# Kernel optimization log

Measured on AMD Instinct MI355X. Metric: run time of the kernel, lower is better.

The kernel has to match this reference:

```python
import jax, jax.numpy as jnp
import numpy as np
from jax import lax

VOCAB = 5000
BLANK = 0          # vocab.unk_id
SMOOTHING = 0.1    # config.model.label_smoothing
ALPHA = 0.2        # config.model.alpha
NEG = -1e30        # finite stand-in for -inf (stable under logaddexp)


def setup_inputs() -> dict:
    key = jax.random.key(0)
    k1, k2, k3 = jax.random.split(key, 3)
    att_logits = jax.random.normal(k1, (16, 128, VOCAB), dtype=jnp.float32)
    ctc_logits = jax.random.normal(k2, (16, 512, VOCAB), dtype=jnp.float32)
    targets = jax.random.randint(k3, (16, 128), 0, VOCAB)
    return {"att_logits": att_logits, "ctc_logits": ctc_logits, "targets": targets}


def _label_smoothing_loss(logit_bsv, targets_bs):
    # torch: label_smoothed filled with smoothing/(V-1), confidence at target;
    # loss = mean over rows of sum(-label_smoothed * logit).
    B, S, V = logit_bsv.shape
    logit = logit_bsv.reshape(-1, V)                       # (B*S, V)
    tgt = targets_bs.reshape(-1)                           # (B*S,)
    confidence = 1.0 - SMOOTHING
    off = SMOOTHING / (V - 1)
    tgt_logit = jnp.take_along_axis(logit, tgt[:, None], axis=1)[:, 0]
    row_sum = jnp.sum(logit, axis=-1)
    # sum(-ls*logit) = -(confidence*logit[t] + off*(row_sum - logit[t]))
    per_row = -(confidence * tgt_logit + off * (row_sum - tgt_logit))
    return jnp.mean(per_row)


def _ctc_loss(log_probs_btv, targets_bs):
    # torch nn.CTCLoss(blank=BLANK, reduction='mean', zero_infinity=True)
    # input is time-major log-probs (T, B, V); full lengths on both sides.
    lp = jnp.transpose(log_probs_btv, (1, 0, 2))           # (T, B, V)
    T, B, V = lp.shape
    S = targets_bs.shape[1]
    L = 2 * S + 1
    # extended target: blank interleaved
    ext = jnp.full((B, L), BLANK, dtype=targets_bs.dtype).at[:, 1::2].set(targets_bs)
    # emission log-probs per extended symbol: (T, B, L)
    emit = jnp.take_along_axis(lp, jnp.broadcast_to(ext[None], (T, B, L)), axis=2)
    # skip (s-2) transition allowed when ext[s] != blank and ext[s] != ext[s-2]
    ext_m2 = jnp.roll(ext, 2, axis=1)
    allow2 = (ext != BLANK) & (ext != ext_m2)
    allow2 = allow2.at[:, :2].set(False)
    alpha0 = jnp.full((B, L), NEG, dtype=lp.dtype)
    alpha0 = alpha0.at[:, 0].set(emit[0, :, 0]).at[:, 1].set(emit[0, :, 1])

    negpad1 = jnp.full((B, 1), NEG, dtype=lp.dtype)
    negpad2 = jnp.full((B, 2), NEG, dtype=lp.dtype)

    def step(alpha, e_t):
        a1 = jnp.concatenate([negpad1, alpha[:, :-1]], axis=1)
        a2 = jnp.concatenate([negpad2, alpha[:, :-2]], axis=1)
        a2 = jnp.where(allow2, a2, NEG)
        new = jnp.logaddexp(jnp.logaddexp(alpha, a1), a2) + e_t
        return new, None

    alphaT, _ = lax.scan(step, alpha0, emit[1:])
    ll = jnp.logaddexp(alphaT[:, L - 1], alphaT[:, L - 2])
    loss_b = -ll                                           # (B,)
    # zero_infinity: invalid paths (loss ~ 1e30) -> 0
    loss_b = jnp.where(loss_b > 1e20, 0.0, loss_b)
    # reduction='mean': divide by target length, then mean over batch
    return jnp.mean(loss_b / S)


def reference(att_logits, ctc_logits, targets):
    att_loss = _label_smoothing_loss(att_logits, targets)
    ctc_loss = _ctc_loss(ctc_logits, targets)
    return ALPHA * att_loss + (1.0 - ALPHA) * ctc_loss
```

## Files before the change

### kernel.cpp

```cpp
#include <hip/hip_runtime.h>
#include <math.h>

#define VOCAB   5000
#define T_CTC   512
#define S_TGT   128
#define BATCH   16
#define ALPHA_W 0.2f
#define CONF    0.9f
#define OFFV    (0.1f / 4999.0f)
#define CSTR    132
#define ATT_N   (BATCH * S_TGT)
#define WS_OFF  4096
#define TCH     16
#define GATHER_BLKS (BATCH * (T_CTC / TCH))

__device__ __forceinline__ double dpp_shr1(double x)
{
    const int lo  = __double2loint(x);
    const int hi  = __double2hiint(x);
    const int slo = __builtin_amdgcn_update_dpp(0, lo, 0x138, 0xF, 0xF, true);
    const int shi = __builtin_amdgcn_update_dpp(0, hi, 0x138, 0xF, 0xF, true);
    return __hiloint2double(shi, slo);
}

__global__ __launch_bounds__(256)
void gather_kernel(const float* __restrict__ ctc, const int* __restrict__ tgt,
                   float* __restrict__ ws)
{
    const int b = blockIdx.x >> 5;
    const int c = blockIdx.x & 31;

    __shared__ int tg[S_TGT];
    if (threadIdx.x < S_TGT) tg[threadIdx.x] = tgt[b * S_TGT + threadIdx.x];
    __syncthreads();

    const float* lp   = ctc + ((size_t)b * T_CTC + (size_t)c * TCH) * VOCAB;
    float*       cbuf = ws + WS_OFF + ((size_t)b * T_CTC + (size_t)c * TCH) * CSTR;

    for (int v = threadIdx.x; v < 258; v += 256) {
        const int tt0 = (v < 129) ? 0 : 1;
        const int idx = (v < 129) ? v : v - 129;
        const int col = (idx < S_TGT) ? tg[idx] : 0;
        float val[TCH / 2];
        #pragma unroll
        for (int p = 0; p < TCH / 2; ++p)
            val[p] = lp[(size_t)(2 * p + tt0) * VOCAB + col];
        #pragma unroll
        for (int p = 0; p < TCH / 2; ++p)
            cbuf[(size_t)(2 * p + tt0) * CSTR + idx] = val[p];
    }
}

__device__ __forceinline__ void prefetch16(const float* __restrict__ cbuf,
                                           int base, int k, float2* E, float* Z)
{
    #pragma unroll
    for (int i = 0; i < 16; ++i) {
        int t = base + i;
        t = (t < T_CTC) ? t : (T_CTC - 1);
        const float* row = cbuf + (size_t)t * CSTR;
        E[i] = *reinterpret_cast<const float2*>(row + 2 * k);
        Z[i] = row[S_TGT];
    }
}

template<bool TAIL>
__device__ __forceinline__ void run16(const float2* E, const float* Z, int base,
                                      double& b0, double& b1, double& b2,
                                      double& b3, double& b4, double& M,
                                      const double g1, const double g3)
{
    #pragma unroll
    for (int i = 0; i < 16; ++i) {
        if (TAIL && (base + i >= T_CTC)) return;
        const float  e0 = Z[i];
        const double X1 = (double)__expf(E[i].x - e0);
        const double X3 = (double)__expf(E[i].y - e0);
        const double p3 = dpp_shr1(b3);
        const double n0 = b0 + p3;
        const double n1 = (b1 + b0 + g1 * p3) * X1;
        const double n2 = b2 + b1;
        const double n3 = (b3 + b2 + g3 * b1) * X3;
        const double n4 = b4 + b3;
        b0 = n0; b1 = n1; b2 = n2; b3 = n3; b4 = n4;
        M += (double)e0;
    }
}

__global__ __launch_bounds__(256, 2)
void ctc_att_kernel(const int* __restrict__ tgt, const float* __restrict__ att,
                    float* __restrict__ ws)
{
    if (blockIdx.x >= BATCH) {
        const int rr = blockIdx.x - BATCH;
        const float* row = att + (size_t)rr * VOCAB;
        const float4* row4 = (const float4*)row;

        float sum = 0.0f;
        for (int i = threadIdx.x; i < VOCAB / 4; i += 256) {
            float4 v = row4[i];
            sum += v.x + v.y + v.z + v.w;
        }
        #pragma unroll
        for (int off = 32; off > 0; off >>= 1)
            sum += __shfl_down(sum, off, 64);

        __shared__ float wsum[4];
        if ((threadIdx.x & 63) == 0) wsum[threadIdx.x >> 6] = sum;
        __syncthreads();
        if (threadIdx.x == 0) {
            const float rs = wsum[0] + wsum[1] + wsum[2] + wsum[3];
            const float tl = row[tgt[rr]];
            ws[rr] = -(CONF * tl + OFFV * (rs - tl));
        }
        return;
    }

    if (threadIdx.x >= 64) return;
    const int b = blockIdx.x;
    const int k = threadIdx.x;
    const int*   tg   = tgt + b * S_TGT;
    const float* cbuf = ws + WS_OFF + (size_t)b * T_CTC * CSTR;

    const int t1 = tg[2 * k];
    const int t3 = tg[2 * k + 1];
    const int tp = (k > 0) ? tg[2 * k - 1] : 0;
    const double g1 = ((k > 0) && (t1 != 0) && (t1 != tp)) ? 1.0 : 0.0;
    const double g3 = ((t3 != 0) && (t3 != t1)) ? 1.0 : 0.0;

    const float e00 = cbuf[S_TGT];
    double M  = (double)e00;
    double b0 = (k == 0) ? 1.0 : 0.0;
    double b1 = (k == 0) ? (double)__expf(cbuf[0] - e00) : 0.0;
    double b2 = 0.0, b3 = 0.0, b4 = 0.0;

    float2 EA[16], EB[16];
    float  ZA[16], ZB[16];

    prefetch16(cbuf, 1, k, EA, ZA);
    for (int h2 = 0; h2 < 16; ++h2) {
        const int base0 = 1 + 32 * h2;
        prefetch16(cbuf, base0 + 16, k, EB, ZB);
        run16<false>(EA, ZA, base0, b0, b1, b2, b3, b4, M, g1, g3);
        if (h2 < 15) {
            prefetch16(cbuf, base0 + 32, k, EA, ZA);
            run16<false>(EB, ZB, base0 + 16, b0, b1, b2, b3, b4, M, g1, g3);
        } else {
            run16<true>(EB, ZB, base0 + 16, b0, b1, b2, b3, b4, M, g1, g3);
        }
    }

    if (k == 63) {
        const double bsum = b3 + b4;
        const double ll   = M + log(bsum);
        float loss_b = (float)(-ll);
        if (!(loss_b <= 1e20f)) loss_b = 0.0f;
        ws[ATT_N + b] = loss_b;
    }
}

__global__ __launch_bounds__(256)
void combine_kernel(const float* __restrict__ ws, float* __restrict__ out)
{
    const int tid = threadIdx.x;
    float s_att = 0.0f;
    for (int i = tid; i < ATT_N; i += 256) s_att += ws[i];
    float s_ctc = (tid < BATCH) ? ws[ATT_N + tid] : 0.0f;

    #pragma unroll
    for (int off = 32; off > 0; off >>= 1) {
        s_att += __shfl_down(s_att, off, 64);
        s_ctc += __shfl_down(s_ctc, off, 64);
    }
    __shared__ float wa[4], wc[4];
    if ((tid & 63) == 0) { wa[tid >> 6] = s_att; wc[tid >> 6] = s_ctc; }
    __syncthreads();
    if (tid == 0) {
        const float inv = 1.0f / (float)ATT_N;
        const float a = (wa[0] + wa[1] + wa[2] + wa[3]) * inv;
        const float c = (wc[0] + wc[1] + wc[2] + wc[3]) * inv;
        out[0] = ALPHA_W * a + (1.0f - ALPHA_W) * c;
    }
}

extern "C" void kernel_launch(void* const* d_in, const int* in_sizes, int n_in,
                              void* d_out, int out_size, void* d_ws, size_t ws_size,
                              hipStream_t stream)
{
    const float* att = (const float*)d_in[0];
    const float* ctc = (const float*)d_in[1];
    const int*   tgt = (const int*)d_in[2];
    float* out = (float*)d_out;
    float* ws  = (float*)d_ws;

    gather_kernel<<<GATHER_BLKS, 256, 0, stream>>>(ctc, tgt, ws);
    ctc_att_kernel<<<BATCH + ATT_N, 256, 0, stream>>>(tgt, att, ws);
    combine_kernel<<<1, 256, 0, stream>>>(ws, out);
}
```

Before: 279.2 us.

## Fuse gather and CTC recurrence into one kernel with per-batch readiness flags

Merges the gather kernel and the CTC/attention kernel into a single launch. Gather blocks come first and signal completion through per-batch atomic counters, and the CTC chain blocks spin on an acquire load until all 32 chunks for their batch are done. This removes a kernel boundary so the attention row sums and the chain setup can overlap with the gather. In exchange it adds a memset launch and relies on lower-indexed blocks being scheduled first to avoid deadlock. It also hoists the target-logit load ahead of the row reduction.

```diff
diff --git a/kernel.cpp b/kernel.cpp
--- a/kernel.cpp
+++ b/kernel.cpp
@@ -13,6 +13,11 @@
 #define WS_OFF  4096
 #define TCH     16
 #define GATHER_BLKS (BATCH * (T_CTC / TCH))
+#define CHAIN_BASE  GATHER_BLKS
+#define ATT_BASE    (CHAIN_BASE + BATCH)
+#define TOTAL_BLKS  (ATT_BASE + ATT_N)
+#define FLAG_IDX    (ATT_N + BATCH)
+#define FLAG_BYTE_OFF (FLAG_IDX * 4)
 
 __device__ __forceinline__ double dpp_shr1(double x)
 {
@@ -21,34 +26,6 @@
     const int slo = __builtin_amdgcn_update_dpp(0, lo, 0x138, 0xF, 0xF, true);
     const int shi = __builtin_amdgcn_update_dpp(0, hi, 0x138, 0xF, 0xF, true);
     return __hiloint2double(shi, slo);
-}
-
-__global__ __launch_bounds__(256)
-void gather_kernel(const float* __restrict__ ctc, const int* __restrict__ tgt,
-                   float* __restrict__ ws)
-{
-    const int b = blockIdx.x >> 5;
-    const int c = blockIdx.x & 31;
-
-    __shared__ int tg[S_TGT];
-    if (threadIdx.x < S_TGT) tg[threadIdx.x] = tgt[b * S_TGT + threadIdx.x];
-    __syncthreads();
-
-    const float* lp   = ctc + ((size_t)b * T_CTC + (size_t)c * TCH) * VOCAB;
-    float*       cbuf = ws + WS_OFF + ((size_t)b * T_CTC + (size_t)c * TCH) * CSTR;
-
-    for (int v = threadIdx.x; v < 258; v += 256) {
-        const int tt0 = (v < 129) ? 0 : 1;
-        const int idx = (v < 129) ? v : v - 129;
-        const int col = (idx < S_TGT) ? tg[idx] : 0;
-        float val[TCH / 2];
-        #pragma unroll
-        for (int p = 0; p < TCH / 2; ++p)
-            val[p] = lp[(size_t)(2 * p + tt0) * VOCAB + col];
-        #pragma unroll
-        for (int p = 0; p < TCH / 2; ++p)
-            cbuf[(size_t)(2 * p + tt0) * CSTR + idx] = val[p];
-    }
 }
 
 __device__ __forceinline__ void prefetch16(const float* __restrict__ cbuf,
@@ -88,16 +65,54 @@
 }
 
 __global__ __launch_bounds__(256, 2)
-void ctc_att_kernel(const int* __restrict__ tgt, const float* __restrict__ att,
-                    float* __restrict__ ws)
-{
-    if (blockIdx.x >= BATCH) {
-        const int rr = blockIdx.x - BATCH;
+void fused_kernel(const float* __restrict__ ctc, const float* __restrict__ att,
+                  const int* __restrict__ tgt, float* __restrict__ ws)
+{
+    const int bid = blockIdx.x;
+    const int tid = threadIdx.x;
+
+    if (bid < GATHER_BLKS) {
+        const int b = bid >> 5;
+        const int c = bid & 31;
+
+        __shared__ int tg[S_TGT];
+        if (tid < S_TGT) tg[tid] = tgt[b * S_TGT + tid];
+        __syncthreads();
+
+        const float* lp   = ctc + ((size_t)b * T_CTC + (size_t)c * TCH) * VOCAB;
+        float*       cbuf = ws + WS_OFF + ((size_t)b * T_CTC + (size_t)c * TCH) * CSTR;
+
+        for (int v = tid; v < 258; v += 256) {
+            const int tt0 = (v < 129) ? 0 : 1;
+            const int idx = (v < 129) ? v : v - 129;
+            const int col = (idx < S_TGT) ? tg[idx] : 0;
+            float val[TCH / 2];
+            #pragma unroll
+            for (int p = 0; p < TCH / 2; ++p)
+                val[p] = lp[(size_t)(2 * p + tt0) * VOCAB + col];
+            #pragma unroll
+            for (int p = 0; p < TCH / 2; ++p)
+                cbuf[(size_t)(2 * p + tt0) * CSTR + idx] = val[p];
+        }
+
+        __syncthreads();
+        if (tid == 0) {
+            __threadfence();
+            atomicAdd((int*)ws + FLAG_IDX + b, 1);
+        }
+        return;
+    }
+
+    if (bid >= ATT_BASE) {
+        const int rr = bid - ATT_BASE;
         const float* row = att + (size_t)rr * VOCAB;
+
+        float tl = 0.0f;
+        if (tid == 0) tl = row[tgt[rr]];
+
         const float4* row4 = (const float4*)row;
-
         float sum = 0.0f;
-        for (int i = threadIdx.x; i < VOCAB / 4; i += 256) {
+        for (int i = tid; i < VOCAB / 4; i += 256) {
             float4 v = row4[i];
             sum += v.x + v.y + v.z + v.w;
         }
@@ -106,19 +121,18 @@
             sum += __shfl_down(sum, off, 64);
 
         __shared__ float wsum[4];
-        if ((threadIdx.x & 63) == 0) wsum[threadIdx.x >> 6] = sum;
+        if ((tid & 63) == 0) wsum[tid >> 6] = sum;
         __syncthreads();
-        if (threadIdx.x == 0) {
+        if (tid == 0) {
             const float rs = wsum[0] + wsum[1] + wsum[2] + wsum[3];
-            const float tl = row[tgt[rr]];
             ws[rr] = -(CONF * tl + OFFV * (rs - tl));
         }
         return;
     }
 
-    if (threadIdx.x >= 64) return;
-    const int b = blockIdx.x;
-    const int k = threadIdx.x;
+    if (tid >= 64) return;
+    const int b = bid - CHAIN_BASE;
+    const int k = tid;
     const int*   tg   = tgt + b * S_TGT;
     const float* cbuf = ws + WS_OFF + (size_t)b * T_CTC * CSTR;
 
@@ -127,6 +141,15 @@
     const int tp = (k > 0) ? tg[2 * k - 1] : 0;
     const double g1 = ((k > 0) && (t1 != 0) && (t1 != tp)) ? 1.0 : 0.0;
     const double g3 = ((t3 != 0) && (t3 != t1)) ? 1.0 : 0.0;
+
+    {
+        int* flag = (int*)ws + FLAG_IDX + b;
+        int r;
+        do {
+            r = __hip_atomic_load(flag, __ATOMIC_ACQUIRE, __HIP_MEMORY_SCOPE_AGENT);
+            if (r != 32) __builtin_amdgcn_s_sleep(8);
+        } while (r != 32);
+    }
 
     const float e00 = cbuf[S_TGT];
     double M  = (double)e00;
@@ -193,7 +216,7 @@
     float* out = (float*)d_out;
     float* ws  = (float*)d_ws;
 
-    gather_kernel<<<GATHER_BLKS, 256, 0, stream>>>(ctc, tgt, ws);
-    ctc_att_kernel<<<BATCH + ATT_N, 256, 0, stream>>>(tgt, att, ws);
+    hipMemsetAsync((char*)ws + FLAG_BYTE_OFF, 0, BATCH * sizeof(int), stream);
+    fused_kernel<<<TOTAL_BLKS, 256, 0, stream>>>(ctc, att, tgt, ws);
     combine_kernel<<<1, 256, 0, stream>>>(ws, out);
 }
```

After: 311.7 us. +11.6%, slower.
